# Optimization experiments

Hardware: AMD Instinct MI355X
Metric: run time of the kernel (lower is better)

## Reference

```python
import jax, jax.numpy as jnp
import numpy as np

N = 100000
E = 1600000
IN_C = 128
OUT_C = 64  # hidden_channels * 2


def setup_inputs() -> dict:
    key = jax.random.key(0)
    k1, k2, k3, k4 = jax.random.split(key, 4)
    x = jax.random.normal(k1, (N, IN_C), dtype=jnp.float32)
    edge_index = jax.random.randint(k2, (2, E), 0, N, dtype=jnp.int64)
    # GCNConv linear weight (stored as [in, out]; equivalent to PyG's lin.weight.T)
    std = 1.0 / np.sqrt(OUT_C)
    weight = jax.random.uniform(k3, (IN_C, OUT_C), dtype=jnp.float32, minval=-std, maxval=std)
    bias = jax.random.uniform(k4, (OUT_C,), dtype=jnp.float32, minval=-std, maxval=std)
    return {"x": x, "edge_index": edge_index, "weight": weight, "bias": bias}


def reference(x, edge_index, weight, bias):
    n = x.shape[0]
    # add self-loops (PyG GCNConv default)
    loops = jnp.arange(n, dtype=edge_index.dtype)
    src = jnp.concatenate([edge_index[0], loops])  # message sources (j)
    dst = jnp.concatenate([edge_index[1], loops])  # aggregation targets (i)

    xw = x @ weight  # [N, OUT_C]

    # symmetric normalization: deg over targets incl. self-loops
    deg = jax.ops.segment_sum(jnp.ones_like(dst, dtype=x.dtype), dst, num_segments=n)
    dinv = jnp.where(deg > 0, jax.lax.rsqrt(deg), 0.0)
    norm = dinv[src] * dinv[dst]  # [E+N]

    msg = xw[src] * norm[:, None]  # gather + scale: [E+N, OUT_C]
    out = jax.ops.segment_sum(msg, dst, num_segments=n)  # scatter-add
    return out + bias
```

## Files before the change

### kernel.cpp

```cpp
#include <hip/hip_runtime.h>
#include <stdint.h>

#define CAP 64
#define CAP_SHIFT 6
#define SUBSZ 196
#define NBUK 512
#define B_E 4096
#define CAPB 20
#define PAIR2_CAP 3840
#define CURS 16

typedef int vint4 __attribute__((ext_vector_type(4)));
typedef float vf32x4 __attribute__((ext_vector_type(4)));
typedef _Float16 vh2 __attribute__((ext_vector_type(2)));
typedef _Float16 vh8 __attribute__((ext_vector_type(8)));

__device__ __forceinline__ unsigned short f2h(float f) {
    _Float16 h = (_Float16)f;
    unsigned short u; __builtin_memcpy(&u, &h, 2); return u;
}
__device__ __forceinline__ unsigned pkadd(unsigned a, unsigned b) {
    vh2 va, vb; __builtin_memcpy(&va, &a, 4); __builtin_memcpy(&vb, &b, 4);
    vh2 r = va + vb;
    unsigned u; __builtin_memcpy(&u, &r, 4); return u;
}
__device__ __forceinline__ float hlo(unsigned u) {
    vh2 v; __builtin_memcpy(&v, &u, 4); return (float)v[0];
}
__device__ __forceinline__ float hhi(unsigned u) {
    vh2 v; __builtin_memcpy(&v, &u, 4); return (float)v[1];
}

__global__ __launch_bounds__(256) void k_part512(const int* __restrict__ eidx, int E,
                                                 unsigned* __restrict__ pairs2,
                                                 int* __restrict__ cursor2) {
    __shared__ unsigned buf[NBUK * CAPB];
    __shared__ int lcnt[NBUK];
    int t = threadIdx.x;
    lcnt[t] = 0; lcnt[t + 256] = 0;
    __syncthreads();

    int base = blockIdx.x * B_E;
    int rem = E - base; if (rem > B_E) rem = B_E;

    auto ins = [&](int s, int d) {
        unsigned sub = (unsigned)d / SUBSZ;
        unsigned wd = ((unsigned)d - sub * SUBSZ) << 17 | (unsigned)s;
        int p = atomicAdd(&lcnt[sub], 1);
        if (p < CAPB) buf[sub * CAPB + p] = wd;
        else {
            int gp = atomicAdd(&cursor2[sub * CURS], 1);
            if (gp < PAIR2_CAP) pairs2[(size_t)sub * PAIR2_CAP + gp] = wd;
        }
    };

    int nvec = rem >> 2;
    const vint4* s4p = (const vint4*)(eidx + base);
    const vint4* d4p = (const vint4*)(eidx + E + base);
    for (int v = t; v < nvec; v += 256) {
        vint4 s4 = __builtin_nontemporal_load(s4p + v);
        vint4 d4 = __builtin_nontemporal_load(d4p + v);
        ins(s4.x, d4.x); ins(s4.y, d4.y); ins(s4.z, d4.z); ins(s4.w, d4.w);
    }
    for (int e = (nvec << 2) + t; e < rem; e += 256)
        ins(eidx[base + e], eidx[E + base + e]);

    __syncthreads();
#pragma unroll
    for (int bo = 0; bo < NBUK; bo += 256) {
        int b = bo + t;
        int c = lcnt[b]; if (c > CAPB) c = CAPB;
        if (c > 0) {
            int gb = atomicAdd(&cursor2[b * CURS], c);
            unsigned* dst = pairs2 + (size_t)b * PAIR2_CAP + gb;
            const unsigned* src = buf + b * CAPB;
            for (int j = 0; j < c; ++j)
                if (gb + j < PAIR2_CAP) dst[j] = src[j];
        }
    }
}

__global__ __launch_bounds__(256) void k_csr(const unsigned* __restrict__ pairs2,
                                             const int* __restrict__ cursor2,
                                             int* __restrict__ cnt,
                                             int* __restrict__ col, int n) {
    __shared__ int lcol[SUBSZ * CAP];
    __shared__ int lcnt[SUBSZ];
    int b = blockIdx.x;
    int node_base = b * SUBSZ;
    int nn = n - node_base; if (nn > SUBSZ) nn = SUBSZ;
    int t = threadIdx.x;
    if (t < SUBSZ) lcnt[t] = 0;
    __syncthreads();

    int len = cursor2[b * CURS]; if (len > PAIR2_CAP) len = PAIR2_CAP;
    const unsigned* p = pairs2 + (size_t)b * PAIR2_CAP;
    for (int j = t; j < len; j += 256) {
        unsigned e = p[j];
        int dsub = e >> 17;
        int s = (int)(e & 0x1FFFFu);
        int pos = atomicAdd(&lcnt[dsub], 1);
        if (pos < CAP - 1) lcol[(dsub << CAP_SHIFT) + 1 + pos] = s;
    }
    __syncthreads();
    if (t < SUBSZ) lcol[t << CAP_SHIFT] = lcnt[t];
    __syncthreads();
    if (nn > 0) {
        vint4* cdst = (vint4*)(col + ((size_t)node_base << CAP_SHIFT));
        const vint4* csrc = (const vint4*)lcol;
        int m = nn * 8;
        for (int j = t; j < m; j += 256) {
            int r = j >> 3, q = j & 7;
            __builtin_nontemporal_store(csrc[r * 16 + q], cdst + r * 16 + q);
        }
        for (int r = t; r < nn; r += 256) {
            if (lcnt[r] > 31) {
#pragma unroll
                for (int q = 8; q < 16; ++q)
                    __builtin_nontemporal_store(csrc[r * 16 + q], cdst + r * 16 + q);
            }
        }
        for (int j = t; j < nn; j += 256)
            cnt[node_base + j] = lcnt[j];
    }
}

__global__ __launch_bounds__(256) void k_gemm(const float* __restrict__ x,
                                              const float* __restrict__ w,
                                              const int* __restrict__ cnt,
                                              unsigned short* __restrict__ xwh, int n) {
    __shared__ unsigned short wT[64 * 128];
    int t = threadIdx.x;
    int row0 = blockIdx.x * 64;

    {
        int c = t & 63;
        int kg = t >> 6;
        const float* wp = w + c;
#pragma unroll
        for (int k2 = 0; k2 < 32; k2 += 2) {
            int k = kg * 32 + k2;
            float f0 = wp[(size_t)k * 64];
            float f1 = wp[(size_t)(k + 1) * 64];
            unsigned pk = (unsigned)f2h(f0) | ((unsigned)f2h(f1) << 16);
            int bo = (c * 256 + k * 2) ^ (((c >> 2) & 7) << 4);
            *(unsigned*)((char*)wT + bo) = pk;
        }
    }
    __syncthreads();

    int lane = t & 63;
    int wid = t >> 6;
    int lr = lane & 15;
    int lg = lane >> 4;
    int rbase = row0 + wid * 16;
    int grow = rbase + lr;
    int gr = grow < n ? grow : 0;
    const float* xr = x + (size_t)gr * 128 + lg * 8;

    vf32x4 acc0 = {0.f,0.f,0.f,0.f}, acc1 = {0.f,0.f,0.f,0.f};
    vf32x4 acc2 = {0.f,0.f,0.f,0.f}, acc3 = {0.f,0.f,0.f,0.f};
#pragma unroll
    for (int ks = 0; ks < 4; ++ks) {
        float4 v0 = *(const float4*)(xr + ks * 32);
        float4 v1 = *(const float4*)(xr + ks * 32 + 4);
        vh8 a;
        a[0] = (_Float16)v0.x; a[1] = (_Float16)v0.y;
        a[2] = (_Float16)v0.z; a[3] = (_Float16)v0.w;
        a[4] = (_Float16)v1.x; a[5] = (_Float16)v1.y;
        a[6] = (_Float16)v1.z; a[7] = (_Float16)v1.w;
        int kb = (ks * 32 + lg * 8) * 2;
        int sw = ((lr & 7) << 4);
        int c0 = 4 * lr,     o0 = (c0 * 256 + kb) ^ sw;
        int c1 = 4 * lr + 1, o1 = (c1 * 256 + kb) ^ sw;
        int c2 = 4 * lr + 2, o2 = (c2 * 256 + kb) ^ sw;
        int c3 = 4 * lr + 3, o3 = (c3 * 256 + kb) ^ sw;
        vh8 b0 = *(const vh8*)((char*)wT + o0);
        vh8 b1 = *(const vh8*)((char*)wT + o1);
        vh8 b2 = *(const vh8*)((char*)wT + o2);
        vh8 b3 = *(const vh8*)((char*)wT + o3);
        acc0 = __builtin_amdgcn_mfma_f32_16x16x32_f16(a, b0, acc0, 0, 0, 0);
        acc1 = __builtin_amdgcn_mfma_f32_16x16x32_f16(a, b1, acc1, 0, 0, 0);
        acc2 = __builtin_amdgcn_mfma_f32_16x16x32_f16(a, b2, acc2, 0, 0, 0);
        acc3 = __builtin_amdgcn_mfma_f32_16x16x32_f16(a, b3, acc3, 0, 0, 0);
    }

    int srow = rbase + lg * 4;
    float dv[4];
#pragma unroll
    for (int r = 0; r < 4; ++r) {
        int row = srow + r;
        int cc = (row < n) ? cnt[row] : 0;
        dv[r] = rsqrtf((float)cc + 1.0f);
    }
#pragma unroll
    for (int r = 0; r < 4; ++r) {
        int row = srow + r;
        if (row < n) {
            ushort4 h = make_ushort4(f2h(acc0[r] * dv[r]), f2h(acc1[r] * dv[r]),
                                     f2h(acc2[r] * dv[r]), f2h(acc3[r] * dv[r]));
            *(ushort4*)&xwh[(size_t)row * 64 + 4 * lr] = h;
        }
    }
}

__global__ __launch_bounds__(256) void k_agg(const int* __restrict__ col,
                                             const unsigned short* __restrict__ xwh,
                                             const float* __restrict__ bias,
                                             float* __restrict__ out, int n) {
    int lane = threadIdx.x & 63;
    int wid  = threadIdx.x >> 6;
    int half = lane >> 5;
    int hl   = lane & 31;
    int i = blockIdx.x * 8 + wid * 2 + half;
    bool valid = i < n;
    int e = lane & 7;
    int g = (lane >> 3) & 3;
    int hbase = lane & 32;

    const int* cp = col + ((size_t)(valid ? i : 0) << CAP_SHIFT);
    int colv = 0;
    if (valid) colv = cp[hl];
    uint4 su = make_uint4(0u, 0u, 0u, 0u);
    if (valid) su = *(const uint4*)(xwh + ((size_t)i << 6) + (e << 3));

    int dr = __shfl(colv, hbase, 64);
    float di = rsqrtf((float)dr + 1.0f);
    int deg = dr < 63 ? dr : 63;
    int deg1 = deg < 31 ? deg : 31;

    unsigned A0 = 0u, A1 = 0u, A2 = 0u, A3 = 0u;
#pragma unroll
    for (int L = 0; L < 8; ++L) {
        int idx = L * 4 + g;
        int j = __shfl(colv, hbase + 1 + (idx < 31 ? idx : 30), 64);
        if (idx < deg1) {
            uint4 u = *(const uint4*)(xwh + ((size_t)j << 6) + (e << 3));
            A0 = pkadd(A0, u.x); A1 = pkadd(A1, u.y);
            A2 = pkadd(A2, u.z); A3 = pkadd(A3, u.w);
        }
    }
    if (__any(dr > 31)) {
        int colv2 = 0;
        if (valid && dr > 31) colv2 = cp[32 + hl];
#pragma unroll
        for (int L = 0; L < 8; ++L) {
            int idx = 31 + L * 4 + g;
            int j = __shfl(colv2, hbase + (L * 4 + g), 64);
            if (idx < deg) {
                uint4 u = *(const uint4*)(xwh + ((size_t)j << 6) + (e << 3));
                A0 = pkadd(A0, u.x); A1 = pkadd(A1, u.y);
                A2 = pkadd(A2, u.z); A3 = pkadd(A3, u.w);
            }
        }
    }
#pragma unroll
    for (int d = 8; d <= 16; d <<= 1) {
        A0 = pkadd(A0, (unsigned)__shfl_xor((int)A0, d, 64));
        A1 = pkadd(A1, (unsigned)__shfl_xor((int)A1, d, 64));
        A2 = pkadd(A2, (unsigned)__shfl_xor((int)A2, d, 64));
        A3 = pkadd(A3, (unsigned)__shfl_xor((int)A3, d, 64));
    }

    if (g == 0 && valid) {
        A0 = pkadd(A0, su.x); A1 = pkadd(A1, su.y);
        A2 = pkadd(A2, su.z); A3 = pkadd(A3, su.w);
        float4 b0 = *(const float4*)(bias + (e << 3));
        float4 b1 = *(const float4*)(bias + (e << 3) + 4);
        vf32x4 o0, o1;
        o0.x = fmaf(hlo(A0), di, b0.x);
        o0.y = fmaf(hhi(A0), di, b0.y);
        o0.z = fmaf(hlo(A1), di, b0.z);
        o0.w = fmaf(hhi(A1), di, b0.w);
        o1.x = fmaf(hlo(A2), di, b1.x);
        o1.y = fmaf(hhi(A2), di, b1.y);
        o1.z = fmaf(hlo(A3), di, b1.z);
        o1.w = fmaf(hhi(A3), di, b1.w);
        float* op = out + ((size_t)i << 6) + (e << 3);
        __builtin_nontemporal_store(o0, (vf32x4*)op);
        __builtin_nontemporal_store(o1, (vf32x4*)(op + 4));
    }
}

extern "C" void kernel_launch(void* const* d_in, const int* in_sizes, int n_in,
                              void* d_out, int out_size, void* d_ws, size_t ws_size,
                              hipStream_t stream) {
    const float* x    = (const float*)d_in[0];
    const int* eidx   = (const int*)d_in[1];
    const float* w    = (const float*)d_in[2];
    const float* bias = (const float*)d_in[3];
    float* out        = (float*)d_out;

    int out_c = in_sizes[3];
    int in_c  = in_sizes[2] / out_c;
    int n     = in_sizes[0] / in_c;
    int E     = in_sizes[1] / 2;

    int nbuk = (n + SUBSZ - 1) / SUBSZ;

    char* ws = (char*)d_ws;
    int*      col = (int*)ws;
    size_t offA = (size_t)n * CAP * 4;
    int*      cnt = (int*)(ws + offA);
    int*      cursor2 = (int*)(ws + offA + (size_t)n * 4);
    char*     baseB = ws + offA + (size_t)n * 4 + (size_t)NBUK * CURS * 4;
    unsigned* pairs2 = (unsigned*)baseB;
    unsigned short* xwh = (unsigned short*)baseB;

    (void)hipMemsetAsync(cursor2, 0, (size_t)NBUK * CURS * 4, stream);
    k_part512<<<(E + B_E - 1) / B_E, 256, 0, stream>>>(eidx, E, pairs2, cursor2);
    k_csr    <<<nbuk, 256, 0, stream>>>(pairs2, cursor2, cnt, col, n);
    k_gemm   <<<(n + 63) / 64, 256, 0, stream>>>(x, w, cnt, xwh, n);
    k_agg    <<<(n + 7) / 8, 256, 0, stream>>>(col, xwh, bias, out, n);
}
```

Measured before the change: 169.5 us.

## Fuse partition and CSR build into one cooperative kernel with grid sync

Merges the memset, edge-partition kernel and per-bucket CSR kernel into a single cooperative launch. The launch uses nbuk blocks with grid-wide syncs between phases, and each block handles E/nbuk edges. This removes two kernel launches and the memset, at the cost of grid.sync overhead. The shared buffer is now sized for the CSR phase, about 50KB, which can limit how many blocks fit per CU. It also relies on all 511 blocks being co-resident, and the cooperative launch fails if they are not.

After: 297.6 us. +75.6%, slower.

```diff
diff --git a/kernel.cpp b/kernel.cpp
--- a/kernel.cpp
+++ b/kernel.cpp
@@ -1,11 +1,13 @@
 #include <hip/hip_runtime.h>
+#include <hip/hip_cooperative_groups.h>
 #include <stdint.h>
+
+namespace cg = cooperative_groups;
 
 #define CAP 64
 #define CAP_SHIFT 6
 #define SUBSZ 196
 #define NBUK 512
-#define B_E 4096
 #define CAPB 20
 #define PAIR2_CAP 3840
 #define CURS 16
@@ -31,22 +33,31 @@
     vh2 v; __builtin_memcpy(&v, &u, 4); return (float)v[1];
 }
 
-__global__ __launch_bounds__(256) void k_part512(const int* __restrict__ eidx, int E,
-                                                 unsigned* __restrict__ pairs2,
-                                                 int* __restrict__ cursor2) {
-    __shared__ unsigned buf[NBUK * CAPB];
-    __shared__ int lcnt[NBUK];
+__global__ __launch_bounds__(256) void k_build(const int* __restrict__ eidx, int E,
+                                               int* __restrict__ cnt,
+                                               int* __restrict__ col,
+                                               unsigned* __restrict__ pairs2,
+                                               int* __restrict__ cursor2,
+                                               int n, int be) {
+    __shared__ __align__(16) char smem[(SUBSZ * CAP + SUBSZ) * 4];
+    cg::grid_group grid = cg::this_grid();
     int t = threadIdx.x;
-    lcnt[t] = 0; lcnt[t + 256] = 0;
-    __syncthreads();
-
-    int base = blockIdx.x * B_E;
-    int rem = E - base; if (rem > B_E) rem = B_E;
+    int bid = blockIdx.x;
+
+    if (t == 0) cursor2[bid * CURS] = 0;
+
+    unsigned* buf = (unsigned*)smem;
+    int* plcnt = (int*)(smem + NBUK * CAPB * 4);
+    plcnt[t] = 0; plcnt[t + 256] = 0;
+    grid.sync();
+
+    int base = bid * be;
+    int rem = E - base; if (rem > be) rem = be; if (rem < 0) rem = 0;
 
     auto ins = [&](int s, int d) {
         unsigned sub = (unsigned)d / SUBSZ;
         unsigned wd = ((unsigned)d - sub * SUBSZ) << 17 | (unsigned)s;
-        int p = atomicAdd(&lcnt[sub], 1);
+        int p = atomicAdd(&plcnt[sub], 1);
         if (p < CAPB) buf[sub * CAPB + p] = wd;
         else {
             int gp = atomicAdd(&cursor2[sub * CURS], 1);
@@ -69,7 +80,7 @@
 #pragma unroll
     for (int bo = 0; bo < NBUK; bo += 256) {
         int b = bo + t;
-        int c = lcnt[b]; if (c > CAPB) c = CAPB;
+        int c = plcnt[b]; if (c > CAPB) c = CAPB;
         if (c > 0) {
             int gb = atomicAdd(&cursor2[b * CURS], c);
             unsigned* dst = pairs2 + (size_t)b * PAIR2_CAP + gb;
@@ -78,32 +89,26 @@
                 if (gb + j < PAIR2_CAP) dst[j] = src[j];
         }
     }
-}
-
-__global__ __launch_bounds__(256) void k_csr(const unsigned* __restrict__ pairs2,
-                                             const int* __restrict__ cursor2,
-                                             int* __restrict__ cnt,
-                                             int* __restrict__ col, int n) {
-    __shared__ int lcol[SUBSZ * CAP];
-    __shared__ int lcnt[SUBSZ];
-    int b = blockIdx.x;
-    int node_base = b * SUBSZ;
+    grid.sync();
+
+    int* lcol = (int*)smem;
+    int* clcnt = (int*)(smem + SUBSZ * CAP * 4);
+    if (t < SUBSZ) clcnt[t] = 0;
+    __syncthreads();
+
+    int node_base = bid * SUBSZ;
     int nn = n - node_base; if (nn > SUBSZ) nn = SUBSZ;
-    int t = threadIdx.x;
-    if (t < SUBSZ) lcnt[t] = 0;
-    __syncthreads();
-
-    int len = cursor2[b * CURS]; if (len > PAIR2_CAP) len = PAIR2_CAP;
-    const unsigned* p = pairs2 + (size_t)b * PAIR2_CAP;
+    int len = cursor2[bid * CURS]; if (len > PAIR2_CAP) len = PAIR2_CAP;
+    const unsigned* p = pairs2 + (size_t)bid * PAIR2_CAP;
     for (int j = t; j < len; j += 256) {
         unsigned e = p[j];
         int dsub = e >> 17;
         int s = (int)(e & 0x1FFFFu);
-        int pos = atomicAdd(&lcnt[dsub], 1);
+        int pos = atomicAdd(&clcnt[dsub], 1);
         if (pos < CAP - 1) lcol[(dsub << CAP_SHIFT) + 1 + pos] = s;
     }
     __syncthreads();
-    if (t < SUBSZ) lcol[t << CAP_SHIFT] = lcnt[t];
+    if (t < SUBSZ) lcol[t << CAP_SHIFT] = clcnt[t];
     __syncthreads();
     if (nn > 0) {
         vint4* cdst = (vint4*)(col + ((size_t)node_base << CAP_SHIFT));
@@ -114,14 +119,14 @@
             __builtin_nontemporal_store(csrc[r * 16 + q], cdst + r * 16 + q);
         }
         for (int r = t; r < nn; r += 256) {
-            if (lcnt[r] > 31) {
+            if (clcnt[r] > 31) {
 #pragma unroll
                 for (int q = 8; q < 16; ++q)
                     __builtin_nontemporal_store(csrc[r * 16 + q], cdst + r * 16 + q);
             }
         }
         for (int j = t; j < nn; j += 256)
-            cnt[node_base + j] = lcnt[j];
+            cnt[node_base + j] = clcnt[j];
     }
 }
 
@@ -297,6 +302,7 @@
     int E     = in_sizes[1] / 2;
 
     int nbuk = (n + SUBSZ - 1) / SUBSZ;
+    int be   = ((E + nbuk - 1) / nbuk + 3) & ~3;
 
     char* ws = (char*)d_ws;
     int*      col = (int*)ws;
@@ -307,9 +313,10 @@
     unsigned* pairs2 = (unsigned*)baseB;
     unsigned short* xwh = (unsigned short*)baseB;
 
-    (void)hipMemsetAsync(cursor2, 0, (size_t)NBUK * CURS * 4, stream);
-    k_part512<<<(E + B_E - 1) / B_E, 256, 0, stream>>>(eidx, E, pairs2, cursor2);
-    k_csr    <<<nbuk, 256, 0, stream>>>(pairs2, cursor2, cnt, col, n);
-    k_gemm   <<<(n + 63) / 64, 256, 0, stream>>>(x, w, cnt, xwh, n);
-    k_agg    <<<(n + 7) / 8, 256, 0, stream>>>(col, xwh, bias, out, n);
-}
+    void* kargs[] = { (void*)&eidx, (void*)&E, (void*)&cnt, (void*)&col,
+                      (void*)&pairs2, (void*)&cursor2, (void*)&n, (void*)&be };
+    (void)hipLaunchCooperativeKernel((void*)k_build, dim3(nbuk), dim3(256),
+                                     kargs, 0, stream);
+    k_gemm<<<(n + 63) / 64, 256, 0, stream>>>(x, w, cnt, xwh, n);
+    k_agg <<<(n + 7) / 8, 256, 0, stream>>>(col, xwh, bias, out, n);
+}
```

## Fuse CSR build and dense GEMM into one kernel per node bucket

Applied to the files above, without the earlier changes.

Merges the CSR-construction kernel and the fp16 MFMA GEMM into a single kernel. Each 196-node bucket block builds its column lists, then reuses the same shared memory for the transposed weight and computes xw for its own nodes, reading degrees straight from shared memory. This drops one launch and the global cnt array write and read. In exchange the GEMM runs over only ~512 blocks, each looping over 13 tiles with 4 waves, and xwh moves to a separate buffer so it no longer aliases pairs2, which costs extra workspace.

Result: no change. 172.2 us (+1.6%).

```diff
diff --git a/kernel.cpp b/kernel.cpp
--- a/kernel.cpp
+++ b/kernel.cpp
@@ -80,15 +80,20 @@
     }
 }
 
-__global__ __launch_bounds__(256) void k_csr(const unsigned* __restrict__ pairs2,
-                                             const int* __restrict__ cursor2,
-                                             int* __restrict__ cnt,
-                                             int* __restrict__ col, int n) {
-    __shared__ int lcol[SUBSZ * CAP];
-    __shared__ int lcnt[SUBSZ];
+__global__ __launch_bounds__(256) void k_csrgemm(const unsigned* __restrict__ pairs2,
+                                                 const int* __restrict__ cursor2,
+                                                 const float* __restrict__ x,
+                                                 const float* __restrict__ w,
+                                                 int* __restrict__ col,
+                                                 unsigned short* __restrict__ xwh,
+                                                 int n) {
+    __shared__ __align__(16) char smem[(SUBSZ * CAP + SUBSZ) * 4];
+    int* lcol = (int*)smem;
+    int* lcnt = (int*)(smem + SUBSZ * CAP * 4);
+    unsigned short* wT = (unsigned short*)smem;
     int b = blockIdx.x;
     int node_base = b * SUBSZ;
-    int nn = n - node_base; if (nn > SUBSZ) nn = SUBSZ;
+    int nn = n - node_base; if (nn > SUBSZ) nn = SUBSZ; if (nn < 0) nn = 0;
     int t = threadIdx.x;
     if (t < SUBSZ) lcnt[t] = 0;
     __syncthreads();
@@ -120,18 +125,8 @@
                     __builtin_nontemporal_store(csrc[r * 16 + q], cdst + r * 16 + q);
             }
         }
-        for (int j = t; j < nn; j += 256)
-            cnt[node_base + j] = lcnt[j];
-    }
-}
-
-__global__ __launch_bounds__(256) void k_gemm(const float* __restrict__ x,
-                                              const float* __restrict__ w,
-                                              const int* __restrict__ cnt,
-                                              unsigned short* __restrict__ xwh, int n) {
-    __shared__ unsigned short wT[64 * 128];
-    int t = threadIdx.x;
-    int row0 = blockIdx.x * 64;
+    }
+    __syncthreads();
 
     {
         int c = t & 63;
@@ -150,56 +145,53 @@
     __syncthreads();
 
     int lane = t & 63;
-    int wid = t >> 6;
+    int wv = t >> 6;
     int lr = lane & 15;
     int lg = lane >> 4;
-    int rbase = row0 + wid * 16;
-    int grow = rbase + lr;
-    int gr = grow < n ? grow : 0;
-    const float* xr = x + (size_t)gr * 128 + lg * 8;
-
-    vf32x4 acc0 = {0.f,0.f,0.f,0.f}, acc1 = {0.f,0.f,0.f,0.f};
-    vf32x4 acc2 = {0.f,0.f,0.f,0.f}, acc3 = {0.f,0.f,0.f,0.f};
-#pragma unroll
-    for (int ks = 0; ks < 4; ++ks) {
-        float4 v0 = *(const float4*)(xr + ks * 32);
-        float4 v1 = *(const float4*)(xr + ks * 32 + 4);
-        vh8 a;
-        a[0] = (_Float16)v0.x; a[1] = (_Float16)v0.y;
-        a[2] = (_Float16)v0.z; a[3] = (_Float16)v0.w;
-        a[4] = (_Float16)v1.x; a[5] = (_Float16)v1.y;
-        a[6] = (_Float16)v1.z; a[7] = (_Float16)v1.w;
-        int kb = (ks * 32 + lg * 8) * 2;
-        int sw = ((lr & 7) << 4);
-        int c0 = 4 * lr,     o0 = (c0 * 256 + kb) ^ sw;
-        int c1 = 4 * lr + 1, o1 = (c1 * 256 + kb) ^ sw;
-        int c2 = 4 * lr + 2, o2 = (c2 * 256 + kb) ^ sw;
-        int c3 = 4 * lr + 3, o3 = (c3 * 256 + kb) ^ sw;
-        vh8 b0 = *(const vh8*)((char*)wT + o0);
-        vh8 b1 = *(const vh8*)((char*)wT + o1);
-        vh8 b2 = *(const vh8*)((char*)wT + o2);
-        vh8 b3 = *(const vh8*)((char*)wT + o3);
-        acc0 = __builtin_amdgcn_mfma_f32_16x16x32_f16(a, b0, acc0, 0, 0, 0);
-        acc1 = __builtin_amdgcn_mfma_f32_16x16x32_f16(a, b1, acc1, 0, 0, 0);
-        acc2 = __builtin_amdgcn_mfma_f32_16x16x32_f16(a, b2, acc2, 0, 0, 0);
-        acc3 = __builtin_amdgcn_mfma_f32_16x16x32_f16(a, b3, acc3, 0, 0, 0);
-    }
-
-    int srow = rbase + lg * 4;
-    float dv[4];
-#pragma unroll
-    for (int r = 0; r < 4; ++r) {
-        int row = srow + r;
-        int cc = (row < n) ? cnt[row] : 0;
-        dv[r] = rsqrtf((float)cc + 1.0f);
-    }
-#pragma unroll
-    for (int r = 0; r < 4; ++r) {
-        int row = srow + r;
-        if (row < n) {
-            ushort4 h = make_ushort4(f2h(acc0[r] * dv[r]), f2h(acc1[r] * dv[r]),
-                                     f2h(acc2[r] * dv[r]), f2h(acc3[r] * dv[r]));
-            *(ushort4*)&xwh[(size_t)row * 64 + 4 * lr] = h;
+    int ntile = (nn + 15) >> 4;
+    for (int tile = wv; tile < ntile; tile += 4) {
+        int rbase = node_base + tile * 16;
+        int grow = rbase + lr;
+        int gr = grow < n ? grow : 0;
+        const float* xr = x + (size_t)gr * 128 + lg * 8;
+
+        vf32x4 acc0 = {0.f,0.f,0.f,0.f}, acc1 = {0.f,0.f,0.f,0.f};
+        vf32x4 acc2 = {0.f,0.f,0.f,0.f}, acc3 = {0.f,0.f,0.f,0.f};
+#pragma unroll
+        for (int ks = 0; ks < 4; ++ks) {
+            float4 v0 = *(const float4*)(xr + ks * 32);
+            float4 v1 = *(const float4*)(xr + ks * 32 + 4);
+            vh8 a;
+            a[0] = (_Float16)v0.x; a[1] = (_Float16)v0.y;
+            a[2] = (_Float16)v0.z; a[3] = (_Float16)v0.w;
+            a[4] = (_Float16)v1.x; a[5] = (_Float16)v1.y;
+            a[6] = (_Float16)v1.z; a[7] = (_Float16)v1.w;
+            int kb = (ks * 32 + lg * 8) * 2;
+            int sw = ((lr & 7) << 4);
+            int c0 = 4 * lr,     o0 = (c0 * 256 + kb) ^ sw;
+            int c1 = 4 * lr + 1, o1 = (c1 * 256 + kb) ^ sw;
+            int c2 = 4 * lr + 2, o2 = (c2 * 256 + kb) ^ sw;
+            int c3 = 4 * lr + 3, o3 = (c3 * 256 + kb) ^ sw;
+            vh8 b0 = *(const vh8*)((char*)wT + o0);
+            vh8 b1 = *(const vh8*)((char*)wT + o1);
+            vh8 b2 = *(const vh8*)((char*)wT + o2);
+            vh8 b3 = *(const vh8*)((char*)wT + o3);
+            acc0 = __builtin_amdgcn_mfma_f32_16x16x32_f16(a, b0, acc0, 0, 0, 0);
+            acc1 = __builtin_amdgcn_mfma_f32_16x16x32_f16(a, b1, acc1, 0, 0, 0);
+            acc2 = __builtin_amdgcn_mfma_f32_16x16x32_f16(a, b2, acc2, 0, 0, 0);
+            acc3 = __builtin_amdgcn_mfma_f32_16x16x32_f16(a, b3, acc3, 0, 0, 0);
+        }
+
+        int sl = tile * 16 + lg * 4;
+#pragma unroll
+        for (int r = 0; r < 4; ++r) {
+            int lrow = sl + r;
+            if (lrow < nn) {
+                float dvv = rsqrtf((float)lcnt[lrow] + 1.0f);
+                ushort4 h = make_ushort4(f2h(acc0[r] * dvv), f2h(acc1[r] * dvv),
+                                         f2h(acc2[r] * dvv), f2h(acc3[r] * dvv));
+                *(ushort4*)&xwh[(size_t)(node_base + lrow) * 64 + 4 * lr] = h;
+            }
         }
     }
 }
@@ -301,15 +293,13 @@
     char* ws = (char*)d_ws;
     int*      col = (int*)ws;
     size_t offA = (size_t)n * CAP * 4;
-    int*      cnt = (int*)(ws + offA);
-    int*      cursor2 = (int*)(ws + offA + (size_t)n * 4);
-    char*     baseB = ws + offA + (size_t)n * 4 + (size_t)NBUK * CURS * 4;
-    unsigned* pairs2 = (unsigned*)baseB;
-    unsigned short* xwh = (unsigned short*)baseB;
+    int*      cursor2 = (int*)(ws + offA);
+    unsigned* pairs2 = (unsigned*)(ws + offA + (size_t)NBUK * CURS * 4);
+    unsigned short* xwh = (unsigned short*)(ws + offA + (size_t)NBUK * CURS * 4
+                                            + (size_t)NBUK * PAIR2_CAP * 4);
 
     (void)hipMemsetAsync(cursor2, 0, (size_t)NBUK * CURS * 4, stream);
     k_part512<<<(E + B_E - 1) / B_E, 256, 0, stream>>>(eidx, E, pairs2, cursor2);
-    k_csr    <<<nbuk, 256, 0, stream>>>(pairs2, cursor2, cnt, col, n);
-    k_gemm   <<<(n + 63) / 64, 256, 0, stream>>>(x, w, cnt, xwh, n);
+    k_csrgemm<<<nbuk, 256, 0, stream>>>(pairs2, cursor2, x, w, col, xwh, n);
     k_agg    <<<(n + 7) / 8, 256, 0, stream>>>(col, xwh, bias, out, n);
 }
```
